# Kernel optimization log

Hardware: AMD Instinct MI355X
Metric: run time of the kernel (lower is better)

## Reference

```python
import jax, jax.numpy as jnp
import numpy as np

ALPHA = 0.2  # leaky_relu negative slope
NEG_INF = -1e9


def setup_inputs() -> dict:
    key = jax.random.key(0)
    ks = jax.random.split(key, 8)
    B, U, N, Din, H, HD = 8, 1024, 2048, 128, 4, 32
    return {
        "user_features": jax.random.normal(ks[0], (B, U, Din), jnp.float32),
        "news_features": jax.random.normal(ks[1], (B, N, Din), jnp.float32),
        "adjacency": jax.random.randint(ks[2], (B, U + N, U + N), 0, 2, jnp.int32),
        "W_user": jax.random.normal(ks[3], (H, Din, HD), jnp.float32) * 0.1,
        "W_news": jax.random.normal(ks[4], (H, Din, HD), jnp.float32) * 0.1,
        "a_user_news": jax.random.normal(ks[5], (H, 2 * HD, 1), jnp.float32) * 0.1,
        "a_news_user": jax.random.normal(ks[6], (H, 2 * HD, 1), jnp.float32) * 0.1,
        "b_user": jnp.zeros((H * HD,), jnp.float32),
        "b_news": jnp.zeros((H * HD,), jnp.float32),
    }


def _attention(q, k, a, mask):
    # q: (B,H,Q,hd), k: (B,H,K,hd), a: (H,2*hd,1), mask: (B,Q,K)
    # Additive score decomposed: [q;k] @ a == q@a_q + k@a_k (same math,
    # avoids materializing the (B,H,Q,K,2hd) concat tensor).
    hd = q.shape[-1]
    a_q = a[:, :hd, 0]  # (H,hd)
    a_k = a[:, hd:, 0]  # (H,hd)
    e_q = jnp.einsum("bhqd,hd->bhq", q, a_q)
    e_k = jnp.einsum("bhkd,hd->bhk", k, a_k)
    scores = e_q[..., :, None] + e_k[..., None, :]  # (B,H,Q,K)
    scores = jnp.where(scores > 0, scores, ALPHA * scores)  # leaky_relu
    scores = jnp.where(mask[:, None, :, :] > 0, scores, NEG_INF)
    return jax.nn.softmax(scores, axis=-1)


def reference(user_features, news_features, adjacency, W_user, W_news,
              a_user_news, a_news_user, b_user, b_news):
    B, U, _ = user_features.shape
    N = news_features.shape[1]
    units = b_user.shape[0]
    user_to_news = adjacency[:, :U, U:]   # (B,U,N)
    news_to_user = adjacency[:, U:, :U]   # (B,N,U)

    q_user = jnp.einsum("bud,hdk->bhuk", user_features, W_user)  # (B,H,U,hd)
    k_news = jnp.einsum("bnd,hdk->bhnk", news_features, W_news)  # (B,H,N,hd)

    attn_un = _attention(q_user, k_news, a_user_news, user_to_news)  # (B,H,U,N)
    user_updates = jnp.einsum("bhun,bhnk->bhuk", attn_un, k_news)

    attn_nu = _attention(k_news, q_user, a_news_user, news_to_user)  # (B,H,N,U)
    news_updates = jnp.einsum("bhnu,bhuk->bhnk", attn_nu, q_user)

    # concat_heads=True: original does a raw reshape of (B,H,*,hd) -> (B,*,units)
    updated_users = jnp.reshape(user_updates, (B, U, units)) + b_user
    updated_news = jnp.reshape(news_updates, (B, N, units)) + b_news
    updated_users = jax.nn.relu(updated_users)
    updated_news = jax.nn.relu(updated_news)
    return updated_users, updated_news
```

## Files before the change

kernel.cpp:

```cpp
#include <hip/hip_runtime.h>
#include <hip/hip_bf16.h>

typedef _Float16 half8 __attribute__((ext_vector_type(8)));
typedef __fp16 fp16x2 __attribute__((ext_vector_type(2)));
typedef float f32x4 __attribute__((ext_vector_type(4)));

#define B_ 8
#define U_ 1024
#define N_ 2048
#define DIN 128
#define H_ 4
#define HD 32
#define S_ 3072
#define LOG2E 1.44269504f

__global__ __launch_bounds__(256) void p1_kernel(
    const float* __restrict__ uf, const float* __restrict__ nf,
    const float* __restrict__ Wu, const float* __restrict__ Wn,
    const float* __restrict__ a_un, const float* __restrict__ a_nu,
    _Float16* __restrict__ vtA, _Float16* __restrict__ vtB,
    float* __restrict__ eRowA, float* __restrict__ eColA,
    float* __restrict__ eRowB, float* __restrict__ eColB)
{
  __shared__ float fs[64][132];
  __shared__ float WsT[32][132];
  __shared__ float qt[32][65];
  __shared__ float aAs[32], aBs[32];

  const int bid = blockIdx.x;
  const int tid = threadIdx.x;

  int b, rt, R;
  const float *feat, *W;
  _Float16* vt;
  float *eA, *eB;
  int aAoff, aBoff;
  const float *avA, *avB;
  if (bid < 128) {
    b = bid >> 4; rt = bid & 15; R = U_;
    feat = uf; W = Wu; vt = vtB;
    eA = eRowA; eB = eColB;
    avA = a_un; aAoff = 0;  avB = a_nu; aBoff = HD;
  } else {
    int t2 = bid - 128;
    b = t2 >> 5; rt = t2 & 31; R = N_;
    feat = nf; W = Wn; vt = vtA;
    eA = eColA; eB = eRowB;
    avA = a_un; aAoff = HD; avB = a_nu; aBoff = 0;
  }
  const int r0 = rt * 64;
  const float4* feat4 = (const float4*)(feat + ((size_t)b * R + r0) * DIN);
  #pragma unroll
  for (int i = 0; i < 8; ++i) {
    int f4 = tid + 256 * i;
    int row = f4 >> 5, c4 = f4 & 31;
    *(float4*)&fs[row][c4 * 4] = feat4[row * 32 + c4];
  }

  const int kk = tid & 15, uu = tid >> 4;
  const int u2 = tid & 63, part = tid >> 6;
  float eAv[H_], eBv[H_];

  #pragma unroll
  for (int h = 0; h < H_; ++h) {
    __syncthreads();
    {
      const float4* W4 = (const float4*)(W + (size_t)h * DIN * HD);
      #pragma unroll
      for (int i = 0; i < 4; ++i) {
        int f4 = tid + 256 * i;
        int d = f4 >> 3, kc = f4 & 7;
        float4 v = W4[f4];
        WsT[kc * 4 + 0][d] = v.x;
        WsT[kc * 4 + 1][d] = v.y;
        WsT[kc * 4 + 2][d] = v.z;
        WsT[kc * 4 + 3][d] = v.w;
      }
      if (tid < 32) {
        aAs[tid] = avA[h * 64 + aAoff + tid];
        aBs[tid] = avB[h * 64 + aBoff + tid];
      }
    }
    __syncthreads();
    {
      float acc0[4] = {0.f, 0.f, 0.f, 0.f}, acc1[4] = {0.f, 0.f, 0.f, 0.f};
      #pragma unroll 8
      for (int d = 0; d < DIN; d += 4) {
        float4 w0 = *(const float4*)&WsT[kk][d];
        float4 w1 = *(const float4*)&WsT[kk + 16][d];
        #pragma unroll
        for (int i = 0; i < 4; ++i) {
          float4 fv = *(const float4*)&fs[uu + 16 * i][d];
          acc0[i] = fmaf(fv.x, w0.x, acc0[i]); acc0[i] = fmaf(fv.y, w0.y, acc0[i]);
          acc0[i] = fmaf(fv.z, w0.z, acc0[i]); acc0[i] = fmaf(fv.w, w0.w, acc0[i]);
          acc1[i] = fmaf(fv.x, w1.x, acc1[i]); acc1[i] = fmaf(fv.y, w1.y, acc1[i]);
          acc1[i] = fmaf(fv.z, w1.z, acc1[i]); acc1[i] = fmaf(fv.w, w1.w, acc1[i]);
        }
      }
      #pragma unroll
      for (int i = 0; i < 4; ++i) {
        qt[kk][uu + 16 * i] = acc0[i];
        qt[kk + 16][uu + 16 * i] = acc1[i];
      }
    }
    __syncthreads();
    {
      size_t vtbase = (size_t)(b * H_ + h) * (R * HD)
                    + (size_t)((r0 >> 5) + (u2 >> 5)) * (HD * 32) + (u2 & 31);
      #pragma unroll
      for (int jj = 0; jj < 8; ++jj) {
        int krow = part * 8 + jj;
        vt[vtbase + krow * 32] = (_Float16)qt[krow][u2];
      }
      float a_ = 0.f, b2_ = 0.f;
      #pragma unroll
      for (int k2 = 0; k2 < HD; ++k2) {
        float qv = qt[k2][u2];
        a_  = fmaf(qv, aAs[k2], a_);
        b2_ = fmaf(qv, aBs[k2], b2_);
      }
      eAv[h] = a_  * LOG2E;
      eBv[h] = b2_ * LOG2E;
    }
  }
  if (part == 0) {
    #pragma unroll
    for (int h = 0; h < H_; ++h)
      eA[(size_t)(b * H_ + h) * R + r0 + u2] = eAv[h];
  } else if (part == 1) {
    #pragma unroll
    for (int h = 0; h < H_; ++h)
      eB[(size_t)(b * H_ + h) * R + r0 + u2] = eBv[h];
  }
}

template<int RR, int CC, int ROFF, int COFF, int PAD64>
__device__ __forceinline__ void p2_core(
    int b, int rt, int wave, int l,
    const int* __restrict__ adj, const _Float16* __restrict__ vt,
    const float* __restrict__ eRow, const float* __restrict__ eCol,
    const float* __restrict__ bias, float* __restrict__ out,
    unsigned long long* maskU)
{
  constexpr int CW64 = CC / 64;

  const int* adjBase = adj + (size_t)b * S_ * S_ + (size_t)(ROFF + rt * 16) * S_ + COFF;
  #pragma unroll 4
  for (int i = 0; i < (16 * CW64) / 4; ++i) {
    int f = i * 4 + wave;
    int row = f / CW64, chunk = f % CW64;
    int av = adjBase[(size_t)row * S_ + chunk * 64 + l];
    unsigned long long m = __ballot(av != 0);
    if (l == 0) maskU[row * PAD64 + chunk] = m;
  }
  __syncthreads();

  const int h = wave;
  const int row16 = l & 15;
  const int cg = (l >> 4) << 3;
  const int r = rt * 16 + row16;
  const float eq = eRow[(size_t)(b * H_ + h) * RR + r];
  const float* ecolH = eCol + (size_t)(b * H_ + h) * CC;
  const _Float16* vtb = vt + (size_t)(b * H_ + h) * (CC * HD);
  const unsigned int* maskW = (const unsigned int*)maskU;
  const int mrow = row16 * (PAD64 * 2);

  f32x4 acc0 = {0.f, 0.f, 0.f, 0.f}, acc1 = {0.f, 0.f, 0.f, 0.f}, accd = {0.f, 0.f, 0.f, 0.f};
  half8 ones = {(_Float16)1.f, (_Float16)1.f, (_Float16)1.f, (_Float16)1.f,
                (_Float16)1.f, (_Float16)1.f, (_Float16)1.f, (_Float16)1.f};

  #pragma unroll 2
  for (int t = 0; t < CC / 32; ++t) {
    const int cb = t * 32 + cg;
    unsigned int mb = maskW[mrow + t] >> cg;
    float4 e0 = *(const float4*)(ecolH + cb);
    float4 e1 = *(const float4*)(ecolH + cb + 4);
    float ecv[8] = {e0.x, e0.y, e0.z, e0.w, e1.x, e1.y, e1.z, e1.w};
    float wv[8];
    #pragma unroll
    for (int j = 0; j < 8; ++j) {
      float s  = eq + ecv[j];
      float ls = fmaxf(s, 0.2f * s);
      ls = (mb & (1u << j)) ? ls : -1e9f;
      wv[j] = exp2f(ls);
    }
    union { fp16x2 h2[4]; half8 h8; } uw;
    #pragma unroll
    for (int j = 0; j < 4; ++j)
      uw.h2[j] = __builtin_amdgcn_cvt_pkrtz(wv[2 * j], wv[2 * j + 1]);
    half8 w = uw.h8;
    const half8 b0 = *(const half8*)(vtb + t * (HD * 32) + row16 * 32 + cg);
    const half8 b1 = *(const half8*)(vtb + t * (HD * 32) + (row16 + 16) * 32 + cg);
    acc0 = __builtin_amdgcn_mfma_f32_16x16x32_f16(w, b0, acc0, 0, 0, 0);
    acc1 = __builtin_amdgcn_mfma_f32_16x16x32_f16(w, b1, acc1, 0, 0, 0);
    accd = __builtin_amdgcn_mfma_f32_16x16x32_f16(w, ones, accd, 0, 0, 0);
  }

  const int colk = row16;
  const int rowbase = rt * 16 + ((l >> 4) << 2);
  #pragma unroll
  for (int q = 0; q < 4; ++q) {
    int orow = rowbase + q;
    size_t o = ((size_t)(b * H_ + h) * RR + orow) * 32 + colk;
    float den = accd[q];
    float v0 = acc0[q] / den + bias[q * 32 + colk];
    float v1 = acc1[q] / den + bias[q * 32 + colk + 16];
    out[o]      = v0 > 0.f ? v0 : 0.f;
    out[o + 16] = v1 > 0.f ? v1 : 0.f;
  }
}

__global__ __launch_bounds__(256, 4) void p2_kernel(
    const int* __restrict__ adj,
    const _Float16* __restrict__ vtA, const _Float16* __restrict__ vtB,
    const float* __restrict__ eRowA, const float* __restrict__ eColA,
    const float* __restrict__ eRowB, const float* __restrict__ eColB,
    const float* __restrict__ bu, const float* __restrict__ bn,
    float* __restrict__ out)
{
  __shared__ unsigned long long maskU[16 * 33];
  const int tid = threadIdx.x;
  const int wave = tid >> 6, l = tid & 63;
  const int bid = blockIdx.x;
  if (bid < B_ * (U_ / 16)) {
    const int b = bid & 7, rt = bid >> 3;
    p2_core<U_, N_, 0, U_, 33>(b, rt, wave, l, adj, vtA, eRowA, eColA, bu,
                               out, maskU);
  } else {
    const int t2 = bid - B_ * (U_ / 16);
    const int b = t2 & 7, rt = t2 >> 3;
    p2_core<N_, U_, U_, 0, 17>(b, rt, wave, l, adj, vtB, eRowB, eColB, bn,
                               out + (size_t)B_ * U_ * 128, maskU);
  }
}

extern "C" void kernel_launch(void* const* d_in, const int* in_sizes, int n_in,
                              void* d_out, int out_size, void* d_ws, size_t ws_size,
                              hipStream_t stream) {
  const float* uf  = (const float*)d_in[0];
  const float* nf  = (const float*)d_in[1];
  const int*   adj = (const int*)d_in[2];
  const float* Wu  = (const float*)d_in[3];
  const float* Wn  = (const float*)d_in[4];
  const float* aun = (const float*)d_in[5];
  const float* anu = (const float*)d_in[6];
  const float* bu  = (const float*)d_in[7];
  const float* bn  = (const float*)d_in[8];

  char* ws = (char*)d_ws;
  size_t off = 0;
  _Float16* vtA = (_Float16*)(ws + off); off += (size_t)B_ * H_ * HD * N_ * 2;
  _Float16* vtB = (_Float16*)(ws + off); off += (size_t)B_ * H_ * HD * U_ * 2;
  float* eRowA = (float*)(ws + off); off += (size_t)B_ * H_ * U_ * 4;
  float* eColA = (float*)(ws + off); off += (size_t)B_ * H_ * N_ * 4;
  float* eRowB = (float*)(ws + off); off += (size_t)B_ * H_ * N_ * 4;
  float* eColB = (float*)(ws + off); off += (size_t)B_ * H_ * U_ * 4;
  (void)off; (void)ws_size; (void)in_sizes; (void)n_in; (void)out_size;

  p1_kernel<<<384, 256, 0, stream>>>(uf, nf, Wu, Wn, aun, anu,
                                     vtA, vtB, eRowA, eColA, eRowB, eColB);
  p2_kernel<<<B_ * (U_ / 16) + B_ * (N_ / 16), 256, 0, stream>>>(
      adj, vtA, vtB, eRowA, eColA, eRowB, eColB, bu, bn, (float*)d_out);
}
```

Before: 119.3 us.

## Split projection blocks per head and process 32 rows per attention block

The projection kernel now launches one block per (batch, row tile, head) instead of looping over heads, which gives it four times the parallelism and removes the per-head barriers. The attention kernel now handles 32 query rows per block, using two row groups of 16 that share the same column-score and value fragment loads. This halves the number of attention blocks and raises the reuse of eCol and V loads. In exchange, projection blocks reload the feature tile once per head, and the larger attention tile uses more registers and a bigger shared-memory mask, which may lower occupancy.

```diff
diff --git a/kernel.cpp b/kernel.cpp
--- a/kernel.cpp
+++ b/kernel.cpp
@@ -30,25 +30,26 @@
   const int bid = blockIdx.x;
   const int tid = threadIdx.x;
 
-  int b, rt, R;
+  int b, rt, R, h;
   const float *feat, *W;
   _Float16* vt;
   float *eA, *eB;
   int aAoff, aBoff;
   const float *avA, *avB;
-  if (bid < 128) {
-    b = bid >> 4; rt = bid & 15; R = U_;
+  if (bid < 512) {
+    h = bid & 3; int t2 = bid >> 2; b = t2 >> 4; rt = t2 & 15; R = U_;
     feat = uf; W = Wu; vt = vtB;
     eA = eRowA; eB = eColB;
     avA = a_un; aAoff = 0;  avB = a_nu; aBoff = HD;
   } else {
-    int t2 = bid - 128;
-    b = t2 >> 5; rt = t2 & 31; R = N_;
+    int t3 = bid - 512;
+    h = t3 & 3; int t2 = t3 >> 2; b = t2 >> 5; rt = t2 & 31; R = N_;
     feat = nf; W = Wn; vt = vtA;
     eA = eColA; eB = eRowB;
     avA = a_un; aAoff = HD; avB = a_nu; aBoff = 0;
   }
   const int r0 = rt * 64;
+
   const float4* feat4 = (const float4*)(feat + ((size_t)b * R + r0) * DIN);
   #pragma unroll
   for (int i = 0; i < 8; ++i) {
@@ -56,81 +57,67 @@
     int row = f4 >> 5, c4 = f4 & 31;
     *(float4*)&fs[row][c4 * 4] = feat4[row * 32 + c4];
   }
+  {
+    const float4* W4 = (const float4*)(W + (size_t)h * DIN * HD);
+    #pragma unroll
+    for (int i = 0; i < 4; ++i) {
+      int f4 = tid + 256 * i;
+      int d = f4 >> 3, kc = f4 & 7;
+      float4 v = W4[f4];
+      WsT[kc * 4 + 0][d] = v.x;
+      WsT[kc * 4 + 1][d] = v.y;
+      WsT[kc * 4 + 2][d] = v.z;
+      WsT[kc * 4 + 3][d] = v.w;
+    }
+    if (tid < 32) {
+      aAs[tid] = avA[h * 64 + aAoff + tid];
+      aBs[tid] = avB[h * 64 + aBoff + tid];
+    }
+  }
+  __syncthreads();
 
   const int kk = tid & 15, uu = tid >> 4;
-  const int u2 = tid & 63, part = tid >> 6;
-  float eAv[H_], eBv[H_];
-
-  #pragma unroll
-  for (int h = 0; h < H_; ++h) {
-    __syncthreads();
-    {
-      const float4* W4 = (const float4*)(W + (size_t)h * DIN * HD);
+  {
+    float acc0[4] = {0.f, 0.f, 0.f, 0.f}, acc1[4] = {0.f, 0.f, 0.f, 0.f};
+    #pragma unroll 8
+    for (int d = 0; d < DIN; d += 4) {
+      float4 w0 = *(const float4*)&WsT[kk][d];
+      float4 w1 = *(const float4*)&WsT[kk + 16][d];
       #pragma unroll
       for (int i = 0; i < 4; ++i) {
-        int f4 = tid + 256 * i;
-        int d = f4 >> 3, kc = f4 & 7;
-        float4 v = W4[f4];
-        WsT[kc * 4 + 0][d] = v.x;
-        WsT[kc * 4 + 1][d] = v.y;
-        WsT[kc * 4 + 2][d] = v.z;
-        WsT[kc * 4 + 3][d] = v.w;
+        float4 fv = *(const float4*)&fs[uu + 16 * i][d];
+        acc0[i] = fmaf(fv.x, w0.x, acc0[i]); acc0[i] = fmaf(fv.y, w0.y, acc0[i]);
+        acc0[i] = fmaf(fv.z, w0.z, acc0[i]); acc0[i] = fmaf(fv.w, w0.w, acc0[i]);
+        acc1[i] = fmaf(fv.x, w1.x, acc1[i]); acc1[i] = fmaf(fv.y, w1.y, acc1[i]);
+        acc1[i] = fmaf(fv.z, w1.z, acc1[i]); acc1[i] = fmaf(fv.w, w1.w, acc1[i]);
       }
-      if (tid < 32) {
-        aAs[tid] = avA[h * 64 + aAoff + tid];
-        aBs[tid] = avB[h * 64 + aBoff + tid];
-      }
-    }
-    __syncthreads();
-    {
-      float acc0[4] = {0.f, 0.f, 0.f, 0.f}, acc1[4] = {0.f, 0.f, 0.f, 0.f};
-      #pragma unroll 8
-      for (int d = 0; d < DIN; d += 4) {
-        float4 w0 = *(const float4*)&WsT[kk][d];
-        float4 w1 = *(const float4*)&WsT[kk + 16][d];
-        #pragma unroll
-        for (int i = 0; i < 4; ++i) {
-          float4 fv = *(const float4*)&fs[uu + 16 * i][d];
-          acc0[i] = fmaf(fv.x, w0.x, acc0[i]); acc0[i] = fmaf(fv.y, w0.y, acc0[i]);
-          acc0[i] = fmaf(fv.z, w0.z, acc0[i]); acc0[i] = fmaf(fv.w, w0.w, acc0[i]);
-          acc1[i] = fmaf(fv.x, w1.x, acc1[i]); acc1[i] = fmaf(fv.y, w1.y, acc1[i]);
-          acc1[i] = fmaf(fv.z, w1.z, acc1[i]); acc1[i] = fmaf(fv.w, w1.w, acc1[i]);
-        }
-      }
-      #pragma unroll
-      for (int i = 0; i < 4; ++i) {
-        qt[kk][uu + 16 * i] = acc0[i];
-        qt[kk + 16][uu + 16 * i] = acc1[i];
-      }
-    }
-    __syncthreads();
-    {
-      size_t vtbase = (size_t)(b * H_ + h) * (R * HD)
-                    + (size_t)((r0 >> 5) + (u2 >> 5)) * (HD * 32) + (u2 & 31);
-      #pragma unroll
-      for (int jj = 0; jj < 8; ++jj) {
-        int krow = part * 8 + jj;
-        vt[vtbase + krow * 32] = (_Float16)qt[krow][u2];
-      }
-      float a_ = 0.f, b2_ = 0.f;
-      #pragma unroll
-      for (int k2 = 0; k2 < HD; ++k2) {
-        float qv = qt[k2][u2];
-        a_  = fmaf(qv, aAs[k2], a_);
-        b2_ = fmaf(qv, aBs[k2], b2_);
-      }
-      eAv[h] = a_  * LOG2E;
-      eBv[h] = b2_ * LOG2E;
-    }
-  }
-  if (part == 0) {
-    #pragma unroll
-    for (int h = 0; h < H_; ++h)
-      eA[(size_t)(b * H_ + h) * R + r0 + u2] = eAv[h];
-  } else if (part == 1) {
-    #pragma unroll
-    for (int h = 0; h < H_; ++h)
-      eB[(size_t)(b * H_ + h) * R + r0 + u2] = eBv[h];
+    }
+    #pragma unroll
+    for (int i = 0; i < 4; ++i) {
+      qt[kk][uu + 16 * i] = acc0[i];
+      qt[kk + 16][uu + 16 * i] = acc1[i];
+    }
+  }
+  __syncthreads();
+
+  const int u2 = tid & 63, part = tid >> 6;
+  {
+    size_t vtbase = (size_t)(b * H_ + h) * (R * HD)
+                  + (size_t)((r0 >> 5) + (u2 >> 5)) * (HD * 32) + (u2 & 31);
+    #pragma unroll
+    for (int jj = 0; jj < 8; ++jj) {
+      int krow = part * 8 + jj;
+      vt[vtbase + krow * 32] = (_Float16)qt[krow][u2];
+    }
+  }
+  if (part < 2) {
+    float a_ = 0.f;
+    const float* av = (part == 0) ? aAs : aBs;
+    #pragma unroll
+    for (int k2 = 0; k2 < HD; ++k2)
+      a_ = fmaf(qt[k2][u2], av[k2], a_);
+    float* e = (part == 0) ? eA : eB;
+    e[(size_t)(b * H_ + h) * R + r0 + u2] = a_ * LOG2E;
   }
 }
 
@@ -144,9 +131,9 @@
 {
   constexpr int CW64 = CC / 64;
 
-  const int* adjBase = adj + (size_t)b * S_ * S_ + (size_t)(ROFF + rt * 16) * S_ + COFF;
+  const int* adjBase = adj + (size_t)b * S_ * S_ + (size_t)(ROFF + rt * 32) * S_ + COFF;
   #pragma unroll 4
-  for (int i = 0; i < (16 * CW64) / 4; ++i) {
+  for (int i = 0; i < (32 * CW64) / 4; ++i) {
     int f = i * 4 + wave;
     int row = f / CW64, chunk = f % CW64;
     int av = adjBase[(size_t)row * S_ + chunk * 64 + l];
@@ -158,53 +145,76 @@
   const int h = wave;
   const int row16 = l & 15;
   const int cg = (l >> 4) << 3;
-  const int r = rt * 16 + row16;
-  const float eq = eRow[(size_t)(b * H_ + h) * RR + r];
+  const int r0 = rt * 32;
+  const float eq0 = eRow[(size_t)(b * H_ + h) * RR + r0 + row16];
+  const float eq1 = eRow[(size_t)(b * H_ + h) * RR + r0 + 16 + row16];
   const float* ecolH = eCol + (size_t)(b * H_ + h) * CC;
   const _Float16* vtb = vt + (size_t)(b * H_ + h) * (CC * HD);
   const unsigned int* maskW = (const unsigned int*)maskU;
-  const int mrow = row16 * (PAD64 * 2);
-
-  f32x4 acc0 = {0.f, 0.f, 0.f, 0.f}, acc1 = {0.f, 0.f, 0.f, 0.f}, accd = {0.f, 0.f, 0.f, 0.f};
+  const int mrow0 = row16 * (PAD64 * 2);
+  const int mrow1 = (row16 + 16) * (PAD64 * 2);
+
+  f32x4 acc00 = {0.f,0.f,0.f,0.f}, acc01 = {0.f,0.f,0.f,0.f}, accd0 = {0.f,0.f,0.f,0.f};
+  f32x4 acc10 = {0.f,0.f,0.f,0.f}, acc11 = {0.f,0.f,0.f,0.f}, accd1 = {0.f,0.f,0.f,0.f};
   half8 ones = {(_Float16)1.f, (_Float16)1.f, (_Float16)1.f, (_Float16)1.f,
                 (_Float16)1.f, (_Float16)1.f, (_Float16)1.f, (_Float16)1.f};
 
   #pragma unroll 2
   for (int t = 0; t < CC / 32; ++t) {
     const int cb = t * 32 + cg;
-    unsigned int mb = maskW[mrow + t] >> cg;
+    unsigned int mb0 = maskW[mrow0 + t] >> cg;
+    unsigned int mb1 = maskW[mrow1 + t] >> cg;
     float4 e0 = *(const float4*)(ecolH + cb);
     float4 e1 = *(const float4*)(ecolH + cb + 4);
     float ecv[8] = {e0.x, e0.y, e0.z, e0.w, e1.x, e1.y, e1.z, e1.w};
-    float wv[8];
+    float wv0[8], wv1[8];
     #pragma unroll
     for (int j = 0; j < 8; ++j) {
-      float s  = eq + ecv[j];
-      float ls = fmaxf(s, 0.2f * s);
-      ls = (mb & (1u << j)) ? ls : -1e9f;
-      wv[j] = exp2f(ls);
-    }
-    union { fp16x2 h2[4]; half8 h8; } uw;
-    #pragma unroll
-    for (int j = 0; j < 4; ++j)
-      uw.h2[j] = __builtin_amdgcn_cvt_pkrtz(wv[2 * j], wv[2 * j + 1]);
-    half8 w = uw.h8;
-    const half8 b0 = *(const half8*)(vtb + t * (HD * 32) + row16 * 32 + cg);
-    const half8 b1 = *(const half8*)(vtb + t * (HD * 32) + (row16 + 16) * 32 + cg);
-    acc0 = __builtin_amdgcn_mfma_f32_16x16x32_f16(w, b0, acc0, 0, 0, 0);
-    acc1 = __builtin_amdgcn_mfma_f32_16x16x32_f16(w, b1, acc1, 0, 0, 0);
-    accd = __builtin_amdgcn_mfma_f32_16x16x32_f16(w, ones, accd, 0, 0, 0);
+      float s0 = eq0 + ecv[j];
+      float s1 = eq1 + ecv[j];
+      float ls0 = fmaxf(s0, 0.2f * s0);
+      float ls1 = fmaxf(s1, 0.2f * s1);
+      ls0 = (mb0 & (1u << j)) ? ls0 : -1e9f;
+      ls1 = (mb1 & (1u << j)) ? ls1 : -1e9f;
+      wv0[j] = exp2f(ls0);
+      wv1[j] = exp2f(ls1);
+    }
+    union { fp16x2 h2[4]; half8 h8; } uw0, uw1;
+    #pragma unroll
+    for (int j = 0; j < 4; ++j) {
+      uw0.h2[j] = __builtin_amdgcn_cvt_pkrtz(wv0[2 * j], wv0[2 * j + 1]);
+      uw1.h2[j] = __builtin_amdgcn_cvt_pkrtz(wv1[2 * j], wv1[2 * j + 1]);
+    }
+    half8 w0 = uw0.h8, w1 = uw1.h8;
+    const half8 vf0 = *(const half8*)(vtb + t * (HD * 32) + row16 * 32 + cg);
+    const half8 vf1 = *(const half8*)(vtb + t * (HD * 32) + (row16 + 16) * 32 + cg);
+    acc00 = __builtin_amdgcn_mfma_f32_16x16x32_f16(w0, vf0, acc00, 0, 0, 0);
+    acc01 = __builtin_amdgcn_mfma_f32_16x16x32_f16(w0, vf1, acc01, 0, 0, 0);
+    accd0 = __builtin_amdgcn_mfma_f32_16x16x32_f16(w0, ones, accd0, 0, 0, 0);
+    acc10 = __builtin_amdgcn_mfma_f32_16x16x32_f16(w1, vf0, acc10, 0, 0, 0);
+    acc11 = __builtin_amdgcn_mfma_f32_16x16x32_f16(w1, vf1, acc11, 0, 0, 0);
+    accd1 = __builtin_amdgcn_mfma_f32_16x16x32_f16(w1, ones, accd1, 0, 0, 0);
   }
 
   const int colk = row16;
-  const int rowbase = rt * 16 + ((l >> 4) << 2);
+  const int g4 = (l >> 4) << 2;
   #pragma unroll
   for (int q = 0; q < 4; ++q) {
-    int orow = rowbase + q;
+    int orow = r0 + g4 + q;
     size_t o = ((size_t)(b * H_ + h) * RR + orow) * 32 + colk;
-    float den = accd[q];
-    float v0 = acc0[q] / den + bias[q * 32 + colk];
-    float v1 = acc1[q] / den + bias[q * 32 + colk + 16];
+    float den = accd0[q];
+    float v0 = acc00[q] / den + bias[q * 32 + colk];
+    float v1 = acc01[q] / den + bias[q * 32 + colk + 16];
+    out[o]      = v0 > 0.f ? v0 : 0.f;
+    out[o + 16] = v1 > 0.f ? v1 : 0.f;
+  }
+  #pragma unroll
+  for (int q = 0; q < 4; ++q) {
+    int orow = r0 + 16 + g4 + q;
+    size_t o = ((size_t)(b * H_ + h) * RR + orow) * 32 + colk;
+    float den = accd1[q];
+    float v0 = acc10[q] / den + bias[q * 32 + colk];
+    float v1 = acc11[q] / den + bias[q * 32 + colk + 16];
     out[o]      = v0 > 0.f ? v0 : 0.f;
     out[o + 16] = v1 > 0.f ? v1 : 0.f;
   }
@@ -218,16 +228,16 @@
     const float* __restrict__ bu, const float* __restrict__ bn,
     float* __restrict__ out)
 {
-  __shared__ unsigned long long maskU[16 * 33];
+  __shared__ unsigned long long maskU[32 * 33];
   const int tid = threadIdx.x;
   const int wave = tid >> 6, l = tid & 63;
   const int bid = blockIdx.x;
-  if (bid < B_ * (U_ / 16)) {
+  if (bid < B_ * (U_ / 32)) {
     const int b = bid & 7, rt = bid >> 3;
     p2_core<U_, N_, 0, U_, 33>(b, rt, wave, l, adj, vtA, eRowA, eColA, bu,
                                out, maskU);
   } else {
-    const int t2 = bid - B_ * (U_ / 16);
+    const int t2 = bid - B_ * (U_ / 32);
     const int b = t2 & 7, rt = t2 >> 3;
     p2_core<N_, U_, U_, 0, 17>(b, rt, wave, l, adj, vtB, eRowB, eColB, bn,
                                out + (size_t)B_ * U_ * 128, maskU);
@@ -257,8 +267,8 @@
   float* eColB = (float*)(ws + off); off += (size_t)B_ * H_ * U_ * 4;
   (void)off; (void)ws_size; (void)in_sizes; (void)n_in; (void)out_size;
 
-  p1_kernel<<<384, 256, 0, stream>>>(uf, nf, Wu, Wn, aun, anu,
-                                     vtA, vtB, eRowA, eColA, eRowB, eColB);
-  p2_kernel<<<B_ * (U_ / 16) + B_ * (N_ / 16), 256, 0, stream>>>(
+  p1_kernel<<<512 + 1024, 256, 0, stream>>>(uf, nf, Wu, Wn, aun, anu,
+                                            vtA, vtB, eRowA, eColA, eRowB, eColB);
+  p2_kernel<<<B_ * (U_ / 32) + B_ * (N_ / 32), 256, 0, stream>>>(
       adj, vtA, vtB, eRowA, eColA, eRowB, eColB, bu, bn, (float*)d_out);
 }
```

Measured after the change: 159.8 us. +34.0%, slower.

## Factor softmax exponentials into precomputed per-column pairs and prefetch tiles

Applied to the files above, without the earlier changes.

Replaces the per-element exp2 of the leaky-relu score with a product of precomputed per-row and per-column exponentials, chosen by a threshold comparison. The column exponentials are stored as float2 pairs by p1. p1 is also split per head to launch more blocks, and the p2 inner loop prefetches the next tile's loads before computing the current one. This trades transcendental work for doubled column-score storage and a risk of overflow or precision loss in the factored exponentials.

```diff
diff --git a/kernel.cpp b/kernel.cpp
--- a/kernel.cpp
+++ b/kernel.cpp
@@ -19,8 +19,8 @@
     const float* __restrict__ Wu, const float* __restrict__ Wn,
     const float* __restrict__ a_un, const float* __restrict__ a_nu,
     _Float16* __restrict__ vtA, _Float16* __restrict__ vtB,
-    float* __restrict__ eRowA, float* __restrict__ eColA,
-    float* __restrict__ eRowB, float* __restrict__ eColB)
+    float* __restrict__ eRowA, float2* __restrict__ eColA2,
+    float* __restrict__ eRowB, float2* __restrict__ eColB2)
 {
   __shared__ float fs[64][132];
   __shared__ float WsT[32][132];
@@ -30,25 +30,28 @@
   const int bid = blockIdx.x;
   const int tid = threadIdx.x;
 
-  int b, rt, R;
+  int b, rt, R, h;
   const float *feat, *W;
   _Float16* vt;
-  float *eA, *eB;
+  float* eRaw;
+  float2* ePair;
+  bool part0raw;
   int aAoff, aBoff;
   const float *avA, *avB;
-  if (bid < 128) {
-    b = bid >> 4; rt = bid & 15; R = U_;
+  if (bid < 512) {
+    h = bid & 3; int t2 = bid >> 2; b = t2 >> 4; rt = t2 & 15; R = U_;
     feat = uf; W = Wu; vt = vtB;
-    eA = eRowA; eB = eColB;
+    eRaw = eRowA; ePair = eColB2; part0raw = true;
     avA = a_un; aAoff = 0;  avB = a_nu; aBoff = HD;
   } else {
-    int t2 = bid - 128;
-    b = t2 >> 5; rt = t2 & 31; R = N_;
+    int t3 = bid - 512;
+    h = t3 & 3; int t2 = t3 >> 2; b = t2 >> 5; rt = t2 & 31; R = N_;
     feat = nf; W = Wn; vt = vtA;
-    eA = eColA; eB = eRowB;
+    eRaw = eRowB; ePair = eColA2; part0raw = false;
     avA = a_un; aAoff = HD; avB = a_nu; aBoff = 0;
   }
   const int r0 = rt * 64;
+
   const float4* feat4 = (const float4*)(feat + ((size_t)b * R + r0) * DIN);
   #pragma unroll
   for (int i = 0; i < 8; ++i) {
@@ -56,89 +59,119 @@
     int row = f4 >> 5, c4 = f4 & 31;
     *(float4*)&fs[row][c4 * 4] = feat4[row * 32 + c4];
   }
+  {
+    const float4* W4 = (const float4*)(W + (size_t)h * DIN * HD);
+    #pragma unroll
+    for (int i = 0; i < 4; ++i) {
+      int f4 = tid + 256 * i;
+      int d = f4 >> 3, kc = f4 & 7;
+      float4 v = W4[f4];
+      WsT[kc * 4 + 0][d] = v.x;
+      WsT[kc * 4 + 1][d] = v.y;
+      WsT[kc * 4 + 2][d] = v.z;
+      WsT[kc * 4 + 3][d] = v.w;
+    }
+    if (tid < 32) {
+      aAs[tid] = avA[h * 64 + aAoff + tid];
+      aBs[tid] = avB[h * 64 + aBoff + tid];
+    }
+  }
+  __syncthreads();
 
   const int kk = tid & 15, uu = tid >> 4;
-  const int u2 = tid & 63, part = tid >> 6;
-  float eAv[H_], eBv[H_];
-
-  #pragma unroll
-  for (int h = 0; h < H_; ++h) {
-    __syncthreads();
-    {
-      const float4* W4 = (const float4*)(W + (size_t)h * DIN * HD);
+  {
+    float acc0[4] = {0.f, 0.f, 0.f, 0.f}, acc1[4] = {0.f, 0.f, 0.f, 0.f};
+    #pragma unroll 8
+    for (int d = 0; d < DIN; d += 4) {
+      float4 w0 = *(const float4*)&WsT[kk][d];
+      float4 w1 = *(const float4*)&WsT[kk + 16][d];
       #pragma unroll
       for (int i = 0; i < 4; ++i) {
-        int f4 = tid + 256 * i;
-        int d = f4 >> 3, kc = f4 & 7;
-        float4 v = W4[f4];
-        WsT[kc * 4 + 0][d] = v.x;
-        WsT[kc * 4 + 1][d] = v.y;
-        WsT[kc * 4 + 2][d] = v.z;
-        WsT[kc * 4 + 3][d] = v.w;
+        float4 fv = *(const float4*)&fs[uu + 16 * i][d];
+        acc0[i] = fmaf(fv.x, w0.x, acc0[i]); acc0[i] = fmaf(fv.y, w0.y, acc0[i]);
+        acc0[i] = fmaf(fv.z, w0.z, acc0[i]); acc0[i] = fmaf(fv.w, w0.w, acc0[i]);
+        acc1[i] = fmaf(fv.x, w1.x, acc1[i]); acc1[i] = fmaf(fv.y, w1.y, acc1[i]);
+        acc1[i] = fmaf(fv.z, w1.z, acc1[i]); acc1[i] = fmaf(fv.w, w1.w, acc1[i]);
       }
-      if (tid < 32) {
-        aAs[tid] = avA[h * 64 + aAoff + tid];
-        aBs[tid] = avB[h * 64 + aBoff + tid];
-      }
-    }
-    __syncthreads();
-    {
-      float acc0[4] = {0.f, 0.f, 0.f, 0.f}, acc1[4] = {0.f, 0.f, 0.f, 0.f};
-      #pragma unroll 8
-      for (int d = 0; d < DIN; d += 4) {
-        float4 w0 = *(const float4*)&WsT[kk][d];
-        float4 w1 = *(const float4*)&WsT[kk + 16][d];
-        #pragma unroll
-        for (int i = 0; i < 4; ++i) {
-          float4 fv = *(const float4*)&fs[uu + 16 * i][d];
-          acc0[i] = fmaf(fv.x, w0.x, acc0[i]); acc0[i] = fmaf(fv.y, w0.y, acc0[i]);
-          acc0[i] = fmaf(fv.z, w0.z, acc0[i]); acc0[i] = fmaf(fv.w, w0.w, acc0[i]);
-          acc1[i] = fmaf(fv.x, w1.x, acc1[i]); acc1[i] = fmaf(fv.y, w1.y, acc1[i]);
-          acc1[i] = fmaf(fv.z, w1.z, acc1[i]); acc1[i] = fmaf(fv.w, w1.w, acc1[i]);
-        }
-      }
-      #pragma unroll
-      for (int i = 0; i < 4; ++i) {
-        qt[kk][uu + 16 * i] = acc0[i];
-        qt[kk + 16][uu + 16 * i] = acc1[i];
-      }
-    }
-    __syncthreads();
-    {
-      size_t vtbase = (size_t)(b * H_ + h) * (R * HD)
-                    + (size_t)((r0 >> 5) + (u2 >> 5)) * (HD * 32) + (u2 & 31);
-      #pragma unroll
-      for (int jj = 0; jj < 8; ++jj) {
-        int krow = part * 8 + jj;
-        vt[vtbase + krow * 32] = (_Float16)qt[krow][u2];
-      }
-      float a_ = 0.f, b2_ = 0.f;
-      #pragma unroll
-      for (int k2 = 0; k2 < HD; ++k2) {
-        float qv = qt[k2][u2];
-        a_  = fmaf(qv, aAs[k2], a_);
-        b2_ = fmaf(qv, aBs[k2], b2_);
-      }
-      eAv[h] = a_  * LOG2E;
-      eBv[h] = b2_ * LOG2E;
-    }
-  }
-  if (part == 0) {
-    #pragma unroll
-    for (int h = 0; h < H_; ++h)
-      eA[(size_t)(b * H_ + h) * R + r0 + u2] = eAv[h];
-  } else if (part == 1) {
-    #pragma unroll
-    for (int h = 0; h < H_; ++h)
-      eB[(size_t)(b * H_ + h) * R + r0 + u2] = eBv[h];
-  }
+    }
+    #pragma unroll
+    for (int i = 0; i < 4; ++i) {
+      qt[kk][uu + 16 * i] = acc0[i];
+      qt[kk + 16][uu + 16 * i] = acc1[i];
+    }
+  }
+  __syncthreads();
+
+  const int u2 = tid & 63, part = tid >> 6;
+  {
+    size_t vtbase = (size_t)(b * H_ + h) * (R * HD)
+                  + (size_t)((r0 >> 5) + (u2 >> 5)) * (HD * 32) + (u2 & 31);
+    #pragma unroll
+    for (int jj = 0; jj < 8; ++jj) {
+      int krow = part * 8 + jj;
+      vt[vtbase + krow * 32] = (_Float16)qt[krow][u2];
+    }
+  }
+  if (part < 2) {
+    float a_ = 0.f;
+    const float* av = (part == 0) ? aAs : aBs;
+    #pragma unroll
+    for (int k2 = 0; k2 < HD; ++k2)
+      a_ = fmaf(qt[k2][u2], av[k2], a_);
+    float e = a_ * LOG2E;
+    size_t idx = (size_t)(b * H_ + h) * R + r0 + u2;
+    bool raw = (part == 0) ? part0raw : !part0raw;
+    if (raw) eRaw[idx] = e;
+    else     ePair[idx] = make_float2(exp2f(e), exp2f(0.2f * e));
+  }
+}
+
+struct Tile { float4 e0, e1, e2, e3; half8 v0, v1; unsigned int mb; };
+
+__device__ __forceinline__ Tile load_tile(
+    int t, int cg, int row16,
+    const float2* __restrict__ ecol2, const _Float16* __restrict__ vtb,
+    const unsigned int* maskW, int mrow)
+{
+  Tile ti;
+  const int cb = t * 32 + cg;
+  const float4* ep = (const float4*)(ecol2 + cb);
+  ti.e0 = ep[0]; ti.e1 = ep[1]; ti.e2 = ep[2]; ti.e3 = ep[3];
+  ti.v0 = *(const half8*)(vtb + t * (HD * 32) + row16 * 32 + cg);
+  ti.v1 = *(const half8*)(vtb + t * (HD * 32) + (row16 + 16) * 32 + cg);
+  ti.mb = maskW[mrow + t] >> cg;
+  return ti;
+}
+
+__device__ __forceinline__ void compute_tile(
+    const Tile& ti, float F1, float F2, float G, half8 ones,
+    f32x4& acc0, f32x4& acc1, f32x4& accd)
+{
+  float wv[8];
+  wv[0] = (ti.mb & 1u)   ? (ti.e0.x > G ? ti.e0.x * F1 : ti.e0.y * F2) : 0.f;
+  wv[1] = (ti.mb & 2u)   ? (ti.e0.z > G ? ti.e0.z * F1 : ti.e0.w * F2) : 0.f;
+  wv[2] = (ti.mb & 4u)   ? (ti.e1.x > G ? ti.e1.x * F1 : ti.e1.y * F2) : 0.f;
+  wv[3] = (ti.mb & 8u)   ? (ti.e1.z > G ? ti.e1.z * F1 : ti.e1.w * F2) : 0.f;
+  wv[4] = (ti.mb & 16u)  ? (ti.e2.x > G ? ti.e2.x * F1 : ti.e2.y * F2) : 0.f;
+  wv[5] = (ti.mb & 32u)  ? (ti.e2.z > G ? ti.e2.z * F1 : ti.e2.w * F2) : 0.f;
+  wv[6] = (ti.mb & 64u)  ? (ti.e3.x > G ? ti.e3.x * F1 : ti.e3.y * F2) : 0.f;
+  wv[7] = (ti.mb & 128u) ? (ti.e3.z > G ? ti.e3.z * F1 : ti.e3.w * F2) : 0.f;
+  union { fp16x2 h2[4]; half8 h8; } uw;
+  uw.h2[0] = __builtin_amdgcn_cvt_pkrtz(wv[0], wv[1]);
+  uw.h2[1] = __builtin_amdgcn_cvt_pkrtz(wv[2], wv[3]);
+  uw.h2[2] = __builtin_amdgcn_cvt_pkrtz(wv[4], wv[5]);
+  uw.h2[3] = __builtin_amdgcn_cvt_pkrtz(wv[6], wv[7]);
+  half8 w = uw.h8;
+  acc0 = __builtin_amdgcn_mfma_f32_16x16x32_f16(w, ti.v0, acc0, 0, 0, 0);
+  acc1 = __builtin_amdgcn_mfma_f32_16x16x32_f16(w, ti.v1, acc1, 0, 0, 0);
+  accd = __builtin_amdgcn_mfma_f32_16x16x32_f16(w, ones, accd, 0, 0, 0);
 }
 
 template<int RR, int CC, int ROFF, int COFF, int PAD64>
 __device__ __forceinline__ void p2_core(
     int b, int rt, int wave, int l,
     const int* __restrict__ adj, const _Float16* __restrict__ vt,
-    const float* __restrict__ eRow, const float* __restrict__ eCol,
+    const float* __restrict__ eRow, const float2* __restrict__ eCol2,
     const float* __restrict__ bias, float* __restrict__ out,
     unsigned long long* maskU)
 {
@@ -160,41 +193,25 @@
   const int cg = (l >> 4) << 3;
   const int r = rt * 16 + row16;
   const float eq = eRow[(size_t)(b * H_ + h) * RR + r];
-  const float* ecolH = eCol + (size_t)(b * H_ + h) * CC;
+  const float F1 = exp2f(eq), F2 = exp2f(0.2f * eq), G = exp2f(-eq);
+  const float2* ecol2 = eCol2 + (size_t)(b * H_ + h) * CC;
   const _Float16* vtb = vt + (size_t)(b * H_ + h) * (CC * HD);
   const unsigned int* maskW = (const unsigned int*)maskU;
   const int mrow = row16 * (PAD64 * 2);
 
-  f32x4 acc0 = {0.f, 0.f, 0.f, 0.f}, acc1 = {0.f, 0.f, 0.f, 0.f}, accd = {0.f, 0.f, 0.f, 0.f};
+  f32x4 acc0 = {0.f,0.f,0.f,0.f}, acc1 = {0.f,0.f,0.f,0.f}, accd = {0.f,0.f,0.f,0.f};
   half8 ones = {(_Float16)1.f, (_Float16)1.f, (_Float16)1.f, (_Float16)1.f,
                 (_Float16)1.f, (_Float16)1.f, (_Float16)1.f, (_Float16)1.f};
 
+  constexpr int T = CC / 32;
+  Tile cur = load_tile(0, cg, row16, ecol2, vtb, maskW, mrow);
   #pragma unroll 2
-  for (int t = 0; t < CC / 32; ++t) {
-    const int cb = t * 32 + cg;
-    unsigned int mb = maskW[mrow + t] >> cg;
-    float4 e0 = *(const float4*)(ecolH + cb);
-    float4 e1 = *(const float4*)(ecolH + cb + 4);
-    float ecv[8] = {e0.x, e0.y, e0.z, e0.w, e1.x, e1.y, e1.z, e1.w};
-    float wv[8];
-    #pragma unroll
-    for (int j = 0; j < 8; ++j) {
-      float s  = eq + ecv[j];
-      float ls = fmaxf(s, 0.2f * s);
-      ls = (mb & (1u << j)) ? ls : -1e9f;
-      wv[j] = exp2f(ls);
-    }
-    union { fp16x2 h2[4]; half8 h8; } uw;
-    #pragma unroll
-    for (int j = 0; j < 4; ++j)
-      uw.h2[j] = __builtin_amdgcn_cvt_pkrtz(wv[2 * j], wv[2 * j + 1]);
-    half8 w = uw.h8;
-    const half8 b0 = *(const half8*)(vtb + t * (HD * 32) + row16 * 32 + cg);
-    const half8 b1 = *(const half8*)(vtb + t * (HD * 32) + (row16 + 16) * 32 + cg);
-    acc0 = __builtin_amdgcn_mfma_f32_16x16x32_f16(w, b0, acc0, 0, 0, 0);
-    acc1 = __builtin_amdgcn_mfma_f32_16x16x32_f16(w, b1, acc1, 0, 0, 0);
-    accd = __builtin_amdgcn_mfma_f32_16x16x32_f16(w, ones, accd, 0, 0, 0);
-  }
+  for (int t = 0; t < T - 1; ++t) {
+    Tile nxt = load_tile(t + 1, cg, row16, ecol2, vtb, maskW, mrow);
+    compute_tile(cur, F1, F2, G, ones, acc0, acc1, accd);
+    cur = nxt;
+  }
+  compute_tile(cur, F1, F2, G, ones, acc0, acc1, accd);
 
   const int colk = row16;
   const int rowbase = rt * 16 + ((l >> 4) << 2);
@@ -213,8 +230,8 @@
 __global__ __launch_bounds__(256, 4) void p2_kernel(
     const int* __restrict__ adj,
     const _Float16* __restrict__ vtA, const _Float16* __restrict__ vtB,
-    const float* __restrict__ eRowA, const float* __restrict__ eColA,
-    const float* __restrict__ eRowB, const float* __restrict__ eColB,
+    const float* __restrict__ eRowA, const float2* __restrict__ eColA2,
+    const float* __restrict__ eRowB, const float2* __restrict__ eColB2,
     const float* __restrict__ bu, const float* __restrict__ bn,
     float* __restrict__ out)
 {
@@ -224,12 +241,12 @@
   const int bid = blockIdx.x;
   if (bid < B_ * (U_ / 16)) {
     const int b = bid & 7, rt = bid >> 3;
-    p2_core<U_, N_, 0, U_, 33>(b, rt, wave, l, adj, vtA, eRowA, eColA, bu,
+    p2_core<U_, N_, 0, U_, 33>(b, rt, wave, l, adj, vtA, eRowA, eColA2, bu,
                                out, maskU);
   } else {
     const int t2 = bid - B_ * (U_ / 16);
     const int b = t2 & 7, rt = t2 >> 3;
-    p2_core<N_, U_, U_, 0, 17>(b, rt, wave, l, adj, vtB, eRowB, eColB, bn,
+    p2_core<N_, U_, U_, 0, 17>(b, rt, wave, l, adj, vtB, eRowB, eColB2, bn,
                                out + (size_t)B_ * U_ * 128, maskU);
   }
 }
@@ -251,14 +268,14 @@
   size_t off = 0;
   _Float16* vtA = (_Float16*)(ws + off); off += (size_t)B_ * H_ * HD * N_ * 2;
   _Float16* vtB = (_Float16*)(ws + off); off += (size_t)B_ * H_ * HD * U_ * 2;
-  float* eRowA = (float*)(ws + off); off += (size_t)B_ * H_ * U_ * 4;
-  float* eColA = (float*)(ws + off); off += (size_t)B_ * H_ * N_ * 4;
-  float* eRowB = (float*)(ws + off); off += (size_t)B_ * H_ * N_ * 4;
-  float* eColB = (float*)(ws + off); off += (size_t)B_ * H_ * U_ * 4;
+  float*  eRowA  = (float*)(ws + off);  off += (size_t)B_ * H_ * U_ * 4;
+  float2* eColA2 = (float2*)(ws + off); off += (size_t)B_ * H_ * N_ * 8;
+  float*  eRowB  = (float*)(ws + off);  off += (size_t)B_ * H_ * N_ * 4;
+  float2* eColB2 = (float2*)(ws + off); off += (size_t)B_ * H_ * U_ * 8;
   (void)off; (void)ws_size; (void)in_sizes; (void)n_in; (void)out_size;
 
-  p1_kernel<<<384, 256, 0, stream>>>(uf, nf, Wu, Wn, aun, anu,
-                                     vtA, vtB, eRowA, eColA, eRowB, eColB);
+  p1_kernel<<<512 + 1024, 256, 0, stream>>>(uf, nf, Wu, Wn, aun, anu,
+                                            vtA, vtB, eRowA, eColA2, eRowB, eColB2);
   p2_kernel<<<B_ * (U_ / 16) + B_ * (N_ / 16), 256, 0, stream>>>(
-      adj, vtA, vtB, eRowA, eColA, eRowB, eColB, bu, bn, (float*)d_out);
-}
+      adj, vtA, vtB, eRowA, eColA2, eRowB, eColB2, bu, bn, (float*)d_out);
+}
```

After: 136.1 us. +14.1%, slower.
